# Performance work log

Hardware: AMD Instinct MI355X
Metric: run time of the kernel (lower is better)

## Reference

```python
import jax, jax.numpy as jnp
import numpy as np

B, S, D = 8, 1024, 768          # batch, block_size, d_model
H = 6                            # n_head
E = 24                           # n_experts
CAP = 4                          # n_expert_capacity
DH = D // H                      # 128, head dim
DF = 384                         # d_ffn
N = S * H                        # tokens after head split = 6144
K = N * CAP // E                 # tokens per expert = 1024


def _uniform(key, shape, fan_in):
    b = 1.0 / np.sqrt(fan_in)
    return jax.random.uniform(key, shape, jnp.float32, -b, b)


def setup_inputs() -> dict:
    key = jax.random.key(0)
    kx, kc, k1, k2, kh, km = jax.random.split(key, 6)
    return {
        "x": jax.random.normal(kx, (B, S, D), jnp.float32),
        "choice": _uniform(kc, (E, DH), DH),
        "w1": _uniform(k1, (E, DH, DF), DH),
        "w2": _uniform(k2, (E, DF, DH), DF),
        "head": _uniform(kh, (D, D), D),
        "merge": _uniform(km, (D, D), D),
    }


def reference(x, choice, w1, w2, head, merge):
    Bb = x.shape[0]
    # input projection then split heads into a token stream of length N
    x = jnp.einsum("bsd,do->bso", x, head)
    x = x.reshape(Bb, N, DH)                              # [B, N, DH]
    # expert-choice routing: softmax over experts per token
    gates = jax.nn.softmax(jnp.einsum("bsd,ed->bse", x, choice), axis=-1)
    # each expert picks its top-K tokens
    G, I = jax.lax.top_k(jnp.swapaxes(gates, -1, -2), K)  # [B, E, K]
    bidx = jnp.arange(Bb)[:, None, None]
    # gather (equivalent to one-hot matmul einsum('beks,bsd->bekd', P, x))
    x_in = x[bidx, I]                                     # [B, E, K, DH]
    # per-expert SwiGLU-free FFN: silu(x w1) w2
    h = jax.nn.silu(jnp.einsum("bekd,edo->beko", x_in, w1))
    x_mlp = jnp.einsum("beki,eid->bekd", h, w2)           # [B, E, K, DH]
    # scatter-combine weighted by gates (einsum('beks,bek,bekd->bsd'))
    x_out = jnp.zeros((Bb, N, DH), x.dtype).at[bidx, I].add(G[..., None] * x_mlp)
    # dropout is identity in eval mode
    x_out = x_out.reshape(Bb, S, D)
    return jnp.einsum("bsd,do->bso", x_out, merge)
```

## Files before the change

kernel.cpp:

```cpp
#include <hip/hip_runtime.h>
#include <stdint.h>
#include <math.h>

typedef __attribute__((ext_vector_type(8))) short short8;
typedef __attribute__((ext_vector_type(4))) short short4v;
typedef __attribute__((ext_vector_type(4))) float floatx4;
typedef __attribute__((ext_vector_type(2))) float floatx2;
typedef __attribute__((ext_vector_type(4))) double double4v;

#define DEV static __device__ __forceinline__

DEV float bf2f(unsigned short u){ union { unsigned int i; float f; } c; c.i = ((unsigned int)u) << 16; return c.f; }
DEV unsigned short f2bf(float f){ union { float f; unsigned int i; } c; c.f = f; unsigned int u = c.i; u += 0x7fffu + ((u >> 16) & 1u); return (unsigned short)(u >> 16); }

#if defined(__has_builtin)
#if __has_builtin(__builtin_amdgcn_global_load_lds)
#define USE_GLL 1
#endif
#if __has_builtin(__builtin_amdgcn_exp2f) && __has_builtin(__builtin_amdgcn_rcpf)
#define FAST_SILU 1
#endif
#endif
#ifndef USE_GLL
#define USE_GLL 0
#endif
#ifndef FAST_SILU
#define FAST_SILU 0
#endif

DEV void gll16(const unsigned short* g, unsigned short* ldsbase, int lane){
#if USE_GLL
  __builtin_amdgcn_global_load_lds((const __attribute__((address_space(1))) void*)g,
                                   (__attribute__((address_space(3))) void*)ldsbase, 16, 0, 0);
#else
  *(short8*)(ldsbase + lane * 8) = *(const short8*)g;
#endif
}

DEV float silu(float v){
#if FAST_SILU
  float ex = __builtin_amdgcn_exp2f(v * -1.44269504088896f);
  return v * __builtin_amdgcn_rcpf(1.f + ex);
#else
  return v / (1.f + __expf(-v));
#endif
}

DEV void transpose_tile(const float* in, unsigned short* out, int R, int C,
                        int bx, int by, int bz, int tid, unsigned short* tile)
{
  const long boff = (long)bz * (long)R * (long)C;
  in += boff; out += boff;
  const int c0 = bx * 64, r0 = by * 64;
  const int rr = tid >> 4;
  const int c4 = (tid & 15) * 4;
#pragma unroll
  for (int i = 0; i < 4; i++){
    int r = rr + i * 16;
    floatx4 v = *(const floatx4*)(in + (long)(r0 + r) * C + c0 + c4);
#pragma unroll
    for (int u = 0; u < 4; u++) tile[r * 68 + c4 + u] = f2bf(v[u]);
  }
  __syncthreads();
#pragma unroll
  for (int i = 0; i < 4; i++){
    int cc = rr + i * 16;
    short4v v;
#pragma unroll
    for (int u = 0; u < 4; u++) v[u] = (short)tile[(c4 + u) * 68 + cc];
    *(short4v*)(out + (long)(c0 + cc) * R + r0 + c4) = v;
  }
}

__global__ __launch_bounds__(256) void k_prep(const float* __restrict__ x,
    const float* __restrict__ choice, const float* __restrict__ w1,
    const float* __restrict__ w2, const float* __restrict__ head,
    const float* __restrict__ merge,
    unsigned short* __restrict__ xb, unsigned short* __restrict__ headT,
    unsigned short* __restrict__ mergeT, unsigned short* __restrict__ w1T,
    unsigned short* __restrict__ w2T, double* __restrict__ W64,
    unsigned int* __restrict__ probe)
{
  __shared__ double buf[1536];
  unsigned short* tile = (unsigned short*)buf;
  const int id = blockIdx.x, tid = threadIdx.x;
  if (id < 144){
    transpose_tile(head, headT, 768, 768, id % 12, id / 12, 0, tid, tile);
  } else if (id < 288){
    int l = id - 144;
    transpose_tile(merge, mergeT, 768, 768, l % 12, l / 12, 0, tid, tile);
  } else if (id < 576){
    int l = id - 288;
    transpose_tile(w1, w1T, 128, 384, l % 6, (l / 6) % 2, l / 12, tid, tile);
  } else if (id < 864){
    int l = id - 576;
    transpose_tile(w2, w2T, 384, 128, l % 2, (l / 2) % 6, l / 12, tid, tile);
  } else if (id < 1248){
    int l = id - 864;
    const int sub = tid >> 7, lt = tid & 127;
    const int d = l * 2 + sub;
    double* hrow = buf + sub * 768;
    for (int i = lt; i < 768; i += 128) hrow[i] = (double)head[(long)d * 768 + i];
    __syncthreads();
    for (int c = lt; c < 144; c += 128){
      int h = c / 24, e = c % 24;
      double a = 0.0;
      const double* hr = hrow + h * 128;
      const float* ch = choice + e * 128;
#pragma unroll 8
      for (int k = 0; k < 128; k++) a += hr[k] * (double)ch[k];
      W64[(long)d * 144 + c] = a;
    }
  } else if (id < 7392){
    const long l = id - 1248;
    const long i = (l * 256 + tid) * 4;
    floatx4 v = *(const floatx4*)(x + i);
    short4v o;
#pragma unroll
    for (int u = 0; u < 4; u++) o[u] = (short)f2bf(v[u]);
    *(short4v*)(xb + i) = o;
  } else {
    if (tid < 64){
      double4v z = {0.0, 0.0, 0.0, 0.0};
      double4v d1 = __builtin_amdgcn_mfma_f64_16x16x4f64((double)tid, 1.0, z, 0, 0, 0);
      double4v d2 = __builtin_amdgcn_mfma_f64_16x16x4f64(1.0, (double)tid, z, 0, 0, 0);
      const int V0 = (int)d1[0];
      const int Astd = ((V0 & 3) == 0) ? 1 : 0;
      unsigned int rp = 0;
      int V;
      V = (int)d1[0]; rp |= (unsigned int)(Astd ? (V - 96) >> 2 : (V - 6) >> 4);
      V = (int)d1[1]; rp |= (unsigned int)(Astd ? (V - 96) >> 2 : (V - 6) >> 4) << 8;
      V = (int)d1[2]; rp |= (unsigned int)(Astd ? (V - 96) >> 2 : (V - 6) >> 4) << 16;
      V = (int)d1[3]; rp |= (unsigned int)(Astd ? (V - 96) >> 2 : (V - 6) >> 4) << 24;
      const int W0 = (int)d2[0];
      const int Bstd = ((W0 & 3) == 0) ? 1 : 0;
      const int cl = Bstd ? (W0 - 96) >> 2 : (W0 - 6) >> 4;
      probe[tid] = rp;
      probe[64 + tid] = (unsigned int)cl;
      if (tid == 0) probe[128] = (unsigned int)(Astd | (Bstd << 1));
    }
  }
}

template<int OUTF>
DEV void gemm_body(const unsigned short* __restrict__ A, const unsigned short* __restrict__ BT,
                   unsigned short* __restrict__ C, float* __restrict__ Cf, int N, int K,
                   unsigned short* As, unsigned short* Bs, int m0, int n0, int tid)
{
  const int lane = tid & 63;
  const int w = tid >> 6;
  const int wy = w >> 1, wx = w & 1;

  floatx4 acc[4][4];
  {
    floatx4 z4 = {0.f, 0.f, 0.f, 0.f};
#pragma unroll
    for (int i = 0; i < 4; i++)
#pragma unroll
      for (int j = 0; j < 4; j++) acc[i][j] = z4;
  }

  const int rsub = lane >> 3;
  const int kcol = (lane & 7) * 8;

  for (int k0 = 0; k0 < K; k0 += 64){
#pragma unroll
    for (int i = 0; i < 4; i++){
      const int inst = w * 4 + i;
      const int rr = inst * 8 + rsub;
      gll16(A + (long)(m0 + rr) * K + k0 + kcol, &As[inst * 512], lane);
      gll16(BT + (long)(n0 + rr) * K + k0 + kcol, &Bs[inst * 512], lane);
    }
    __syncthreads();
#pragma unroll
    for (int ks = 0; ks < 2; ++ks){
      const int kb = ks * 32 + (lane >> 4) * 8;
      short8 af[4], bfr[4];
#pragma unroll
      for (int mi = 0; mi < 4; mi++) af[mi]  = *(const short8*)&As[(wy * 64 + mi * 16 + (lane & 15)) * 64 + kb];
#pragma unroll
      for (int ni = 0; ni < 4; ni++) bfr[ni] = *(const short8*)&Bs[(wx * 64 + ni * 16 + (lane & 15)) * 64 + kb];
#pragma unroll
      for (int mi = 0; mi < 4; mi++)
#pragma unroll
        for (int ni = 0; ni < 4; ni++)
          acc[mi][ni] = __builtin_amdgcn_mfma_f32_16x16x32_bf16(af[mi], bfr[ni], acc[mi][ni], 0, 0, 0);
    }
    __syncthreads();
  }

  const int ml = lane & 15;
  const int rq = (lane >> 4) * 4;
#pragma unroll
  for (int mi = 0; mi < 4; mi++){
    const int rowb = m0 + wy * 64 + mi * 16 + rq;
#pragma unroll
    for (int ni = 0; ni < 4; ni++){
      const int col = n0 + wx * 64 + ni * 16 + ml;
#pragma unroll
      for (int r = 0; r < 4; r++){
        float v = acc[mi][ni][r];
        if (OUTF) Cf[(long)(rowb + r) * N + col] = v;
        else      C[(long)(rowb + r) * N + col] = f2bf(v);
      }
    }
  }
}

DEV void gates_mfma(const float* __restrict__ xg, const double* __restrict__ W,
                    double* __restrict__ P, const unsigned int* __restrict__ probe,
                    int id, int tid)
{
  const int lane = tid & 63, w = tid >> 6;
  const unsigned int flags = probe[128];
  const int Astd = (int)(flags & 1u), Bstd = (int)((flags >> 1) & 1u);
  const unsigned int rp = probe[lane];
  const int cl = (int)probe[64 + lane];
  const int ar = Astd ? (lane & 15) : (lane >> 2);
  const int ak = Astd ? (lane >> 4) : (lane & 3);
  const int bk = Bstd ? (lane >> 4) : (lane & 3);
  const int bj = Bstd ? (lane & 15) : (lane >> 2);

  const int kseg = id >> 7;
  const int row0 = (id & 127) * 64 + w * 16;

  double4v acc[9];
#pragma unroll
  for (int t = 0; t < 9; t++) acc[t] = (double4v){0.0, 0.0, 0.0, 0.0};

  const float* arow = xg + (long)(row0 + ar) * 768;
  const int kbase = kseg * 192;
  for (int kc = 0; kc < 192; kc += 4){
    const int k0 = kbase + kc;
    const double a = (double)arow[k0 + ak];
    const double* wr = W + (long)(k0 + bk) * 144 + bj;
#pragma unroll
    for (int t = 0; t < 9; t++)
      acc[t] = __builtin_amdgcn_mfma_f64_16x16x4f64(a, wr[t * 16], acc[t], 0, 0, 0);
  }

  const int r0_ = (int)(rp & 255u), r1_ = (int)((rp >> 8) & 255u);
  const int r2_ = (int)((rp >> 16) & 255u), r3_ = (int)((rp >> 24) & 255u);
  double* dst = P + (long)kseg * 8192 * 144 + (long)row0 * 144;
#pragma unroll
  for (int t = 0; t < 9; t++){
    const int cb = t * 16 + cl;
    dst[(long)r0_ * 144 + cb] = acc[t][0];
    dst[(long)r1_ * 144 + cb] = acc[t][1];
    dst[(long)r2_ * 144 + cb] = acc[t][2];
    dst[(long)r3_ * 144 + cb] = acc[t][3];
  }
}

__global__ __launch_bounds__(256, 4) void k_main0(const unsigned short* __restrict__ xb,
    const unsigned short* __restrict__ headT, unsigned short* __restrict__ x1,
    const float* __restrict__ xg, const double* __restrict__ W, double* __restrict__ P,
    const unsigned int* __restrict__ probe)
{
  __shared__ unsigned short lds[128 * 64 * 2];
  const int id = blockIdx.x, tid = threadIdx.x;
  if (id < 512){
    gates_mfma(xg, W, P, probe, id, tid);
  } else {
    const int id2 = id - 512;
    unsigned short* As = lds;
    unsigned short* Bs = As + 128 * 64;
    gemm_body<0>(xb, headT, x1, nullptr, 768, 768, As, Bs, (id2 & 63) * 128, (id2 >> 6) * 128, tid);
  }
}

__global__ __launch_bounds__(256) void k_softmax(const double* __restrict__ P,
                                                 double* __restrict__ gatesT)
{
  const int gid = blockIdx.x * 256 + threadIdx.x;
  const int R = gid / 6, h = gid % 6;
  const int b = R >> 10, s = R & 1023;
  const int n = s * 6 + h;
  const long S = (long)8192 * 144;
  const long base = (long)R * 144 + h * 24;
  double l[24];
#pragma unroll
  for (int e = 0; e < 24; e++){
    const long o = base + e;
    l[e] = (P[o] + P[S + o]) + (P[2 * S + o] + P[3 * S + o]);
  }
  double m = l[0];
#pragma unroll
  for (int e = 1; e < 24; e++) m = fmax(m, l[e]);
  double ssum = 0.0;
#pragma unroll
  for (int e = 0; e < 24; e++){ l[e] = exp(l[e] - m); ssum += l[e]; }
  double is = 1.0 / ssum;
#pragma unroll
  for (int e = 0; e < 24; e++)
    gatesT[((long)(b * 24 + e)) * 6144 + n] = l[e] * is;
}

DEV int blk_reduce(int v, volatile int* sbuf, int tid){
#pragma unroll
  for (int off = 32; off > 0; off >>= 1) v += __shfl_down(v, off);
  __syncthreads();
  if ((tid & 63) == 0) sbuf[tid >> 6] = v;
  __syncthreads();
  return sbuf[0] + sbuf[1] + sbuf[2] + sbuf[3];
}

__global__ __launch_bounds__(256) void k_topk(const double* __restrict__ gatesT,
                                              int* __restrict__ Kidx, float* __restrict__ Gval,
                                              int* __restrict__ cnt, unsigned short* __restrict__ inv)
{
  __shared__ int sbuf[4];
  __shared__ int s_pos;
  const int tid = threadIdx.x;
  const int be = blockIdx.x;
  const int b = be / 24, e = be % 24;
  const double* g = gatesT + (long)be * 6144;

  unsigned long long key[24];
#pragma unroll
  for (int j = 0; j < 24; j++)
    key[j] = (unsigned long long)__double_as_longlong(g[tid + 256 * j]);

  unsigned long long lo = 0ull, hi = ~0ull;
  for (int it = 0; it < 64; ++it){
    if (hi - lo <= 1ull) break;
    unsigned long long mid = lo + ((hi - lo) >> 1);
    int c = 0;
#pragma unroll
    for (int j = 0; j < 24; j++) c += (key[j] > mid) ? 1 : 0;
    c = blk_reduce(c, sbuf, tid);
    if (c >= 1024) lo = mid; else hi = mid;
  }
  const unsigned long long T = hi;
  int cg = 0;
#pragma unroll
  for (int j = 0; j < 24; j++) cg += (key[j] > T) ? 1 : 0;
  cg = blk_reduce(cg, sbuf, tid);
  const int need = 1024 - cg;

  int lo2 = 0, hi2 = 6144;
  for (int it = 0; it < 13; ++it){
    if (hi2 - lo2 <= 1) break;
    int mid = (lo2 + hi2) >> 1;
    int c = 0;
#pragma unroll
    for (int j = 0; j < 24; j++) c += (key[j] == T && (tid + 256 * j) < mid) ? 1 : 0;
    c = blk_reduce(c, sbuf, tid);
    if (c >= need) hi2 = mid; else lo2 = mid;
  }
  const int m = hi2;

  if (tid == 0) s_pos = 0;
  __syncthreads();
#pragma unroll
  for (int j = 0; j < 24; j++){
    int n = tid + 256 * j;
    bool sel = (key[j] > T) || (key[j] == T && n < m);
    if (sel){
      int slot = atomicAdd(&s_pos, 1);
      Kidx[(long)be * 1024 + slot] = n;
      Gval[(long)be * 1024 + slot] = (float)__longlong_as_double((long long)key[j]);
      int t = b * 6144 + n;
      int p = atomicAdd(&cnt[t], 1);
      inv[(long)t * 24 + p] = (unsigned short)(e * 1024 + slot);
    }
  }
}

__global__ __launch_bounds__(256, 2) void k_gemm2(const unsigned short* __restrict__ A,
    const unsigned short* __restrict__ BT, float* __restrict__ Cf)
{
  __shared__ unsigned short As[128 * 64];
  __shared__ unsigned short Bs[128 * 64];
  gemm_body<1>(A, BT, nullptr, Cf, 768, 768, As, Bs,
               (int)blockIdx.x * 128, (int)blockIdx.y * 128, (int)threadIdx.x);
}

__global__ __launch_bounds__(256, 4) void k_ffn(const unsigned short* __restrict__ x1,
    const unsigned short* __restrict__ w1T, const unsigned short* __restrict__ w2T,
    const int* __restrict__ KidxAll, const float* __restrict__ GvalAll,
    unsigned short* __restrict__ Y)
{
  __shared__ unsigned short W1c[2][64 * 128];
  __shared__ unsigned short Hc[64 * 64];
  const int tid = threadIdx.x, lane = tid & 63, w = tid >> 6;
  const int tx = lane & 15, quad = lane >> 4;
  const int mt = blockIdx.x;
  const int be = blockIdx.y;
  const int b = be / 24, e = be % 24;
  const int* idx = KidxAll + (long)be * 1024 + mt * 64;
  const float* scl = GvalAll + (long)be * 1024 + mt * 64;
  const unsigned short* A   = x1  + (long)b * 6144 * 128;
  const unsigned short* w1e = w1T + (long)e * 384 * 128;
  const unsigned short* w2e = w2T + (long)e * 128 * 384;

  short8 afr[4];
  {
    const int r0 = idx[w * 16 + tx];
    const unsigned short* a0 = A + (long)r0 * 128 + quad * 8;
#pragma unroll
    for (int ks = 0; ks < 4; ks++) afr[ks] = *(const short8*)(a0 + ks * 32);
  }

  floatx4 Yt[2][4];
  {
    floatx4 z4 = {0.f, 0.f, 0.f, 0.f};
#pragma unroll
    for (int i = 0; i < 2; i++)
#pragma unroll
      for (int j = 0; j < 4; j++) Yt[i][j] = z4;
  }

  const unsigned short* w2b = w2e + (long)(w * 32 + tx) * 384 + quad * 8;

  {
    const int r0 = w * 16;
#pragma unroll
    for (int i = 0; i < 4; i++){
      int lr = r0 + i * 4 + quad;
      int c = tx ^ (lr & 15);
      gll16(w1e + (long)lr * 128 + c * 8, &W1c[0][(r0 + i * 4) * 128], lane);
    }
  }

  for (int nc = 0; nc < 6; ++nc){
    const int cur = nc & 1;
    __syncthreads();

    if (nc < 5){
      const int r0 = w * 16;
#pragma unroll
      for (int i = 0; i < 4; i++){
        int lr = r0 + i * 4 + quad;
        int c = tx ^ (lr & 15);
        gll16(w1e + (long)((nc + 1) * 64 + lr) * 128 + c * 8, &W1c[cur ^ 1][(r0 + i * 4) * 128], lane);
      }
    }

    short8 a2[2][2];
    {
      const unsigned short* wb = w2b + nc * 64;
#pragma unroll
      for (int ks = 0; ks < 2; ++ks)
#pragma unroll
        for (int mf = 0; mf < 2; ++mf)
          a2[ks][mf] = *(const short8*)(wb + (long)mf * 16 * 384 + ks * 32);
    }

    floatx4 h4[4];
    {
      floatx4 z4 = {0.f, 0.f, 0.f, 0.f};
#pragma unroll
      for (int j = 0; j < 4; j++) h4[j] = z4;
    }
#pragma unroll
    for (int ks = 0; ks < 4; ++ks){
      const int chunk = ks * 4 + quad;
      const int pos = chunk ^ tx;
#pragma unroll
      for (int nf = 0; nf < 4; ++nf){
        short8 bfr = *(const short8*)&W1c[cur][(nf * 16 + tx) * 128 + pos * 8];
        h4[nf] = __builtin_amdgcn_mfma_f32_16x16x32_bf16(afr[ks], bfr, h4[nf], 0, 0, 0);
      }
    }
#pragma unroll
    for (int nf = 0; nf < 4; ++nf){
      const int hchunk = nf * 2 + (tx >> 3);
      const int hoff = tx & 7;
#pragma unroll
      for (int r = 0; r < 4; r++){
        float v = silu(h4[nf][r]);
        const int trow = w * 16 + quad * 4 + r;
        Hc[trow * 64 + (hchunk ^ (trow & 7)) * 8 + hoff] = f2bf(v);
      }
    }
    __syncthreads();

#pragma unroll
    for (int ks = 0; ks < 2; ++ks){
      const int chunk2 = ks * 4 + quad;
      const int posx = chunk2 ^ (tx & 7);
      short8 b2[4];
#pragma unroll
      for (int nf = 0; nf < 4; ++nf)
        b2[nf] = *(const short8*)&Hc[(nf * 16 + tx) * 64 + posx * 8];
#pragma unroll
      for (int mf = 0; mf < 2; ++mf)
#pragma unroll
        for (int nf = 0; nf < 4; ++nf)
          Yt[mf][nf] = __builtin_amdgcn_mfma_f32_16x16x32_bf16(a2[ks][mf], b2[nf], Yt[mf][nf], 0, 0, 0);
    }
  }

#pragma unroll
  for (int nf = 0; nf < 4; ++nf){
    const int rb = nf * 16 + tx;
    const float g = scl[rb];
    unsigned short* dst = Y + ((long)be * 1024 + mt * 64 + rb) * 128 + w * 32 + quad * 4;
#pragma unroll
    for (int mf = 0; mf < 2; ++mf){
      short4v v;
#pragma unroll
      for (int r = 0; r < 4; r++) v[r] = (short)f2bf(Yt[mf][nf][r] * g);
      *(short4v*)(dst + mf * 16) = v;
    }
  }
}

__global__ __launch_bounds__(256) void k_combine(const int* __restrict__ cnt,
    const unsigned short* __restrict__ inv, const unsigned short* __restrict__ Y,
    unsigned short* __restrict__ xout)
{
  const int t = blockIdx.x * 4 + (threadIdx.x >> 6);
  const int lane = threadIdx.x & 63;
  const int b = t / 6144;
  const int c = cnt[t];
  float a0 = 0.f, a1 = 0.f;
  for (int p = 0; p < c; ++p){
    int code = inv[(long)t * 24 + p];
    int e = code >> 10, slot = code & 1023;
    const unsigned short* y = Y + (((long)(b * 24 + e) * 1024 + slot) << 7) + lane * 2;
    a0 += bf2f(y[0]); a1 += bf2f(y[1]);
  }
  unsigned short* o = xout + ((long)t << 7) + lane * 2;
  o[0] = f2bf(a0); o[1] = f2bf(a1);
}

extern "C" void kernel_launch(void* const* d_in, const int* in_sizes, int n_in,
                              void* d_out, int out_size, void* d_ws, size_t ws_size,
                              hipStream_t stream)
{
  const float* x      = (const float*)d_in[0];
  const float* choice = (const float*)d_in[1];
  const float* w1     = (const float*)d_in[2];
  const float* w2     = (const float*)d_in[3];
  const float* head   = (const float*)d_in[4];
  const float* merge  = (const float*)d_in[5];
  float* out = (float*)d_out;
  (void)in_sizes; (void)n_in; (void)out_size; (void)ws_size;

  char* p = (char*)d_ws;
  auto alloc = [&p](size_t bytes) -> void* {
    void* q = (void*)p; p += (bytes + 255) & ~(size_t)255; return q;
  };

  unsigned short* headT = (unsigned short*)alloc((size_t)768 * 768 * 2);
  unsigned short* mergeT= (unsigned short*)alloc((size_t)768 * 768 * 2);
  unsigned short* w1T   = (unsigned short*)alloc((size_t)24 * 384 * 128 * 2);
  unsigned short* w2T   = (unsigned short*)alloc((size_t)24 * 128 * 384 * 2);
  double* W64           = (double*)alloc((size_t)768 * 144 * 8);
  int* Kidx             = (int*)alloc((size_t)192 * 1024 * 4);
  float* Gval           = (float*)alloc((size_t)192 * 1024 * 4);
  int* cnt              = (int*)alloc((size_t)49152 * 4);
  unsigned short* inv   = (unsigned short*)alloc((size_t)49152 * 24 * 2);
  unsigned short* xb    = (unsigned short*)alloc((size_t)8192 * 768 * 2);
  unsigned short* x1    = (unsigned short*)alloc((size_t)8192 * 768 * 2);
  unsigned short* Y     = (unsigned short*)alloc((size_t)192 * 1024 * 128 * 2);
  double* P             = (double*)Y;
  double* gatesT        = (double*)((char*)Y + (size_t)4 * 8192 * 144 * 8);
  unsigned short* xout  = xb;
  unsigned int* probe   = (unsigned int*)Kidx;

  hipMemsetAsync(cnt, 0, (size_t)49152 * 4, stream);
  k_prep<<<dim3(7393), 256, 0, stream>>>(x, choice, w1, w2, head, merge,
                                         xb, headT, mergeT, w1T, w2T, W64, probe);
  k_main0<<<dim3(896), 256, 0, stream>>>(xb, headT, x1, x, W64, P, probe);
  k_softmax<<<dim3(192), 256, 0, stream>>>(P, gatesT);
  k_topk<<<dim3(192), 256, 0, stream>>>(gatesT, Kidx, Gval, cnt, inv);
  k_ffn<<<dim3(16, 192, 1), 256, 0, stream>>>(x1, w1T, w2T, Kidx, Gval, Y);
  k_combine<<<dim3(12288), 256, 0, stream>>>(cnt, inv, Y, xout);
  k_gemm2<<<dim3(64, 6, 1), 256, 0, stream>>>(xout, mergeT, out);
}
```

Measured before the change: 348.0 us.

## Repartition expert FFN second GEMM per wave to drop intra-iteration barrier

The second GEMM of the expert FFN is re-split so that each wave computes all 128 output columns for its own 16 tokens, instead of 32 columns for all 64 tokens. Each wave then reads back only the rows of the hidden-activation LDS buffer it wrote itself, which lets the __syncthreads between writing and reading that buffer be removed. In exchange, every wave now loads the whole per-chunk w2 slice from global memory rather than a quarter of it. That multiplies w2 traffic per block by four and raises register pressure from the extra w2 fragments loaded inside the loop.

Result: slower. 436.5 us (+25.4%).

```diff
diff --git a/kernel.cpp b/kernel.cpp
--- a/kernel.cpp
+++ b/kernel.cpp
@@ -402,16 +402,12 @@
     for (int ks = 0; ks < 4; ks++) afr[ks] = *(const short8*)(a0 + ks * 32);
   }
 
-  floatx4 Yt[2][4];
+  floatx4 Yt[8];
   {
     floatx4 z4 = {0.f, 0.f, 0.f, 0.f};
 #pragma unroll
-    for (int i = 0; i < 2; i++)
-#pragma unroll
-      for (int j = 0; j < 4; j++) Yt[i][j] = z4;
-  }
-
-  const unsigned short* w2b = w2e + (long)(w * 32 + tx) * 384 + quad * 8;
+    for (int i = 0; i < 8; i++) Yt[i] = z4;
+  }
 
   {
     const int r0 = w * 16;
@@ -426,7 +422,6 @@
   for (int nc = 0; nc < 6; ++nc){
     const int cur = nc & 1;
     __syncthreads();
-
     if (nc < 5){
       const int r0 = w * 16;
 #pragma unroll
@@ -437,16 +432,6 @@
       }
     }
 
-    short8 a2[2][2];
-    {
-      const unsigned short* wb = w2b + nc * 64;
-#pragma unroll
-      for (int ks = 0; ks < 2; ++ks)
-#pragma unroll
-        for (int mf = 0; mf < 2; ++mf)
-          a2[ks][mf] = *(const short8*)(wb + (long)mf * 16 * 384 + ks * 32);
-    }
-
     floatx4 h4[4];
     {
       floatx4 z4 = {0.f, 0.f, 0.f, 0.f};
@@ -474,35 +459,28 @@
         Hc[trow * 64 + (hchunk ^ (trow & 7)) * 8 + hoff] = f2bf(v);
       }
     }
-    __syncthreads();
 
 #pragma unroll
     for (int ks = 0; ks < 2; ++ks){
-      const int chunk2 = ks * 4 + quad;
-      const int posx = chunk2 ^ (tx & 7);
-      short8 b2[4];
-#pragma unroll
-      for (int nf = 0; nf < 4; ++nf)
-        b2[nf] = *(const short8*)&Hc[(nf * 16 + tx) * 64 + posx * 8];
-#pragma unroll
-      for (int mf = 0; mf < 2; ++mf)
-#pragma unroll
-        for (int nf = 0; nf < 4; ++nf)
-          Yt[mf][nf] = __builtin_amdgcn_mfma_f32_16x16x32_bf16(a2[ks][mf], b2[nf], Yt[mf][nf], 0, 0, 0);
-    }
-  }
-
-#pragma unroll
-  for (int nf = 0; nf < 4; ++nf){
-    const int rb = nf * 16 + tx;
-    const float g = scl[rb];
-    unsigned short* dst = Y + ((long)be * 1024 + mt * 64 + rb) * 128 + w * 32 + quad * 4;
-#pragma unroll
-    for (int mf = 0; mf < 2; ++mf){
+      short8 b2 = *(const short8*)&Hc[(w * 16 + tx) * 64 + (((ks * 4 + quad) ^ (tx & 7)) * 8)];
+      const unsigned short* wb = w2e + (long)tx * 384 + nc * 64 + ks * 32 + quad * 8;
+#pragma unroll
+      for (int mi = 0; mi < 8; ++mi){
+        short8 a2 = *(const short8*)(wb + (long)mi * 16 * 384);
+        Yt[mi] = __builtin_amdgcn_mfma_f32_16x16x32_bf16(a2, b2, Yt[mi], 0, 0, 0);
+      }
+    }
+  }
+
+  {
+    const float g = scl[w * 16 + tx];
+    unsigned short* dst = Y + ((long)be * 1024 + mt * 64 + w * 16 + tx) * 128 + quad * 4;
+#pragma unroll
+    for (int mi = 0; mi < 8; ++mi){
       short4v v;
 #pragma unroll
-      for (int r = 0; r < 4; r++) v[r] = (short)f2bf(Yt[mf][nf][r] * g);
-      *(short4v*)(dst + mf * 16) = v;
+      for (int r = 0; r < 4; r++) v[r] = (short)f2bf(Yt[mi][r] * g);
+      *(short4v*)(dst + mi * 16) = v;
     }
   }
 }
```
